# Performance work log

Hardware: AMD Instinct MI355X
Metric: run time of the kernel (lower is better)

## Reference

```python
import jax, jax.numpy as jnp
import numpy as np
import math

N, T, D = 4096, 32, 158
NEWS, DGRU = 1024, 128
G, E, H, K = 8, 8, 4, 2          # groups, experts/group, heads, top_k
HID = G * E                       # 64
DH = E // H                       # head_dim = 2
NEG = -1e30


def setup_inputs() -> dict:
    key = jax.random.key(0)
    ks = jax.random.split(key, 16)
    s = 0.05
    price_feature = jax.random.normal(ks[0], (N, T, D), jnp.float32)
    news_feature = jax.random.normal(ks[1], (N, T, NEWS), jnp.float32)
    news_mask = jax.random.uniform(ks[2], (N, T), dtype=jnp.float32)
    # simple deterministic router params (stand-in for injected router module)
    router_W = jax.random.normal(ks[3], (D + NEWS, DGRU), jnp.float32) * s
    router_b = jnp.zeros((DGRU,), jnp.float32)
    # hidden_to_gate: Linear(d_gru -> hidden_dim)
    gate_W = jax.random.normal(ks[4], (DGRU, HID), jnp.float32) * s
    gate_b = jnp.zeros((HID,), jnp.float32)
    # 64 tiny experts: Linear(hidden_dim -> 1), stacked [G,E,HID]
    expert_W = jax.random.normal(ks[5], (G, E, HID), jnp.float32) * s
    expert_b = jnp.zeros((G, E), jnp.float32)
    # per-group attention weights, torch Linear layout [out,in] -> [G,E,E]
    wq = jax.random.normal(ks[6], (G, E, E), jnp.float32) * s
    wk = jax.random.normal(ks[7], (G, E, E), jnp.float32) * s
    wv = jax.random.normal(ks[8], (G, E, E), jnp.float32) * s
    wo = jax.random.normal(ks[9], (G, E, E), jnp.float32) * s
    wq_b = jnp.zeros((G, E), jnp.float32)
    wk_b = jnp.zeros((G, E), jnp.float32)
    wv_b = jnp.zeros((G, E), jnp.float32)
    wo_b = jnp.zeros((G, E), jnp.float32)
    return dict(price_feature=price_feature, news_feature=news_feature, news_mask=news_mask,
                router_W=router_W, router_b=router_b, gate_W=gate_W, gate_b=gate_b,
                expert_W=expert_W, expert_b=expert_b,
                wq=wq, wq_b=wq_b, wk=wk, wk_b=wk_b, wv=wv, wv_b=wv_b, wo=wo, wo_b=wo_b)


def _forward(price_feature, news_feature, news_mask, router_W, router_b,
             gate_W, gate_b, expert_W, expert_b,
             wq, wq_b, wk, wk_b, wv, wv_b, wo, wo_b):
    n = price_feature.shape[0]
    # ---- router: masked temporal pooling + linear + tanh -> [N, d_gru]
    m = news_mask[:, :, None]
    news_agg = (news_feature * m).sum(1) / jnp.clip(m.sum(1), 1e-6)
    price_agg = price_feature.mean(1)
    h = jnp.tanh(jnp.concatenate([price_agg, news_agg], axis=-1) @ router_W + router_b)
    # ---- gate: [N, HID]
    hidden = h @ gate_W + gate_b
    # ---- top-k routing with scatter mask + masked softmax
    top_k_values, top_k_indices = jax.lax.top_k(hidden, K)
    mask = jnp.zeros_like(hidden).at[jnp.arange(n)[:, None], top_k_indices].set(1.0)
    masked_hidden = jnp.where(mask == 0, NEG, hidden)
    routing_weights = jax.nn.softmax(masked_hidden, axis=1)  # [N, HID]
    # ---- all 64 experts at once: [N, G, E]
    expert_out = jnp.einsum('nh,geh->nge', hidden, expert_W) + expert_b
    # ---- inner-group attention (faithful to torch view/transpose layout)
    q = jnp.einsum('nge,gfe->ngf', expert_out, wq) + wq_b
    k = jnp.einsum('nge,gfe->ngf', expert_out, wk) + wk_b
    v = jnp.einsum('nge,gfe->ngf', expert_out, wv) + wv_b
    # view [N,G,H,DH] then transpose(1,2) -> attend over DH positions, H as features
    qt = q.reshape(n, G, H, DH).transpose(0, 1, 3, 2)  # [N,G,DH,H]
    kt = k.reshape(n, G, H, DH).transpose(0, 1, 3, 2)
    vt = v.reshape(n, G, H, DH).transpose(0, 1, 3, 2)
    scores = jnp.einsum('ngdh,ngeh->ngde', qt, kt) / math.sqrt(DH)  # [N,G,DH,DH]
    attn = jax.nn.softmax(scores, axis=-1)
    attended = jnp.einsum('ngde,ngeh->ngdh', attn, vt)  # [N,G,DH,H]
    attended = attended.transpose(0, 1, 3, 2).reshape(n, G, E)
    agg = jnp.einsum('nge,gfe->ngf', attended, wo) + wo_b  # [N,G,E]
    all_outputs = agg.reshape(n, HID)
    weighted = all_outputs * routing_weights
    predictions = weighted.sum(axis=1)  # [N]
    return predictions, routing_weights, hidden, top_k_indices, routing_weights


def reference(price_feature, news_feature, news_mask, router_W, router_b,
              gate_W, gate_b, expert_W, expert_b,
              wq, wq_b, wk, wk_b, wv, wv_b, wo, wo_b):
    return _forward(price_feature, news_feature, news_mask, router_W, router_b,
                    gate_W, gate_b, expert_W, expert_b,
                    wq, wq_b, wk, wk_b, wv, wv_b, wo, wo_b)
```

## Files before the change

### kernel.cpp

```cpp
#include <hip/hip_runtime.h>
#include <math.h>

namespace {

constexpr int TT    = 32;
constexpr int DD    = 158;
constexpr int NEWSC = 1024;
constexpr int XDIM  = 1182;
constexpr int XPAD  = 1184;
constexpr int DGRU  = 128;
constexpr int HIDN  = 64;
constexpr int RPB   = 8;
constexpr int SPLIT = 592;

__global__ __launch_bounds__(256, 2)
void miga_fused(const float* __restrict__ price,
                const float* __restrict__ news,
                const float* __restrict__ mask,
                const float* __restrict__ rW,
                const float* __restrict__ rb,
                const float* __restrict__ gW,
                const float* __restrict__ gb,
                const float* __restrict__ eW,
                const float* __restrict__ eb,
                const float* __restrict__ wq,
                const float* __restrict__ wqb,
                const float* __restrict__ wk,
                const float* __restrict__ wkb,
                const float* __restrict__ wv,
                const float* __restrict__ wvb,
                const float* __restrict__ wo,
                const float* __restrict__ wob,
                float* __restrict__ out, int nrows)
{
  __shared__ __align__(16) float xs[RPB][XPAD];
  __shared__ float hs[RPB][DGRU];
  __shared__ float part[RPB][DGRU];
  __shared__ float hid_s[RPB][HIDN];
  __shared__ float eo_s[RPB][HIDN];
  __shared__ float q_s[RPB][HIDN];
  __shared__ float k_s[RPB][HIDN];
  __shared__ float v_s[RPB][HIDN];
  __shared__ float att_s[RPB][HIDN];
  __shared__ float den_m[RPB];

  float* eWt = &xs[0][0];

  const int tid  = threadIdx.x;
  const int row0 = blockIdx.x * RPB;

  if (tid < RPB) {
    float s = 0.f;
    #pragma unroll
    for (int t = 0; t < TT; ++t) s += mask[(size_t)(row0 + tid) * TT + t];
    den_m[tid] = fmaxf(s, 1e-6f);
  }

  if (tid < DD) {
    for (int r = 0; r < RPB; ++r) {
      const float* pr = price + ((size_t)(row0 + r) * TT) * DD + tid;
      float acc = 0.f;
      #pragma unroll
      for (int t = 0; t < TT; ++t) acc += pr[(size_t)t * DD];
      xs[r][tid] = acc * (1.0f / (float)TT);
    }
  }
  __syncthreads();

  {
    const int j0 = tid * 4;
    for (int r = 0; r < RPB; ++r) {
      const float* nb = news + ((size_t)(row0 + r) * TT) * NEWSC + j0;
      const float* mb = mask + (size_t)(row0 + r) * TT;
      float ax = 0.f, ay = 0.f, az = 0.f, aw = 0.f;
      #pragma unroll 4
      for (int t = 0; t < TT; ++t) {
        const float  mv = mb[t];
        const float4 nv = *(const float4*)(nb + (size_t)t * NEWSC);
        ax += mv * nv.x; ay += mv * nv.y; az += mv * nv.z; aw += mv * nv.w;
      }
      const float dn = den_m[r];
      xs[r][DD + j0 + 0] = ax / dn;
      xs[r][DD + j0 + 1] = ay / dn;
      xs[r][DD + j0 + 2] = az / dn;
      xs[r][DD + j0 + 3] = aw / dn;
    }
  }
  __syncthreads();

  {
    const int sh = tid >> 7;
    const int o  = tid & 127;
    const int ib = sh ? SPLIT : 0;
    const int ie = sh ? XDIM : SPLIT;
    float acc[RPB];
    #pragma unroll
    for (int r = 0; r < RPB; ++r) acc[r] = 0.f;
    int i0 = ib;
    for (; i0 + 8 <= ie; i0 += 8) {
      const float w0 = rW[(size_t)(i0 + 0) * DGRU + o];
      const float w1 = rW[(size_t)(i0 + 1) * DGRU + o];
      const float w2 = rW[(size_t)(i0 + 2) * DGRU + o];
      const float w3 = rW[(size_t)(i0 + 3) * DGRU + o];
      const float w4 = rW[(size_t)(i0 + 4) * DGRU + o];
      const float w5 = rW[(size_t)(i0 + 5) * DGRU + o];
      const float w6 = rW[(size_t)(i0 + 6) * DGRU + o];
      const float w7 = rW[(size_t)(i0 + 7) * DGRU + o];
      #pragma unroll
      for (int r = 0; r < RPB; ++r) {
        const float4 xa = *(const float4*)&xs[r][i0];
        const float4 xb = *(const float4*)&xs[r][i0 + 4];
        acc[r] += xa.x * w0 + xa.y * w1 + xa.z * w2 + xa.w * w3
                + xb.x * w4 + xb.y * w5 + xb.z * w6 + xb.w * w7;
      }
    }
    for (; i0 < ie; ++i0) {
      const float w = rW[(size_t)i0 * DGRU + o];
      #pragma unroll
      for (int r = 0; r < RPB; ++r) acc[r] += xs[r][i0] * w;
    }
    if (sh) {
      #pragma unroll
      for (int r = 0; r < RPB; ++r) part[r][o] = acc[r];
    }
    __syncthreads();
    if (!sh) {
      const float b = rb[o];
      #pragma unroll
      for (int r = 0; r < RPB; ++r) hs[r][o] = tanhf(acc[r] + part[r][o] + b);
    }
    #pragma unroll
    for (int kk = 0; kk < 16; ++kk) {
      const int f  = tid + 256 * kk;
      const int ge = f >> 6;
      const int j  = f & 63;
      eWt[j * 65 + ge] = eW[f];
    }
  }
  __syncthreads();

  const int wgi = tid >> 6;
  const int ln  = tid & 63;
  const int ra  = wgi;
  const int rb2 = wgi + 4;

  float h0 = gb[ln], h1 = gb[ln];
  #pragma unroll 4
  for (int i = 0; i < DGRU; ++i) {
    const float w = gW[(size_t)i * HIDN + ln];
    h0 += hs[ra][i]  * w;
    h1 += hs[rb2][i] * w;
  }
  hid_s[ra][ln]  = h0;
  hid_s[rb2][ln] = h1;
  __syncthreads();

  float* out_pred = out;
  float* out_rw1  = out + (size_t)nrows;
  float* out_hid  = out + (size_t)nrows * 65;
  float* out_idx  = out + (size_t)nrows * 129;
  float* out_rw2  = out + (size_t)nrows * 131;

  const float hvv[2] = {h0, h1};
  int   i1v[2], i2v[2];
  float w1v[2], w2v[2];
  #pragma unroll
  for (int rr = 0; rr < 2; ++rr) {
    const int r   = wgi + rr * 4;
    const int row = row0 + r;
    const float hv = hvv[rr];
    float bv = hv; int bi = ln;
    #pragma unroll
    for (int off = 32; off >= 1; off >>= 1) {
      const float ov = __shfl_xor(bv, off);
      const int   oi = __shfl_xor(bi, off);
      if (ov > bv || (ov == bv && oi < bi)) { bv = ov; bi = oi; }
    }
    float cv = (ln == bi) ? -1e30f : hv; int ci = ln;
    #pragma unroll
    for (int off = 32; off >= 1; off >>= 1) {
      const float ov = __shfl_xor(cv, off);
      const int   oi = __shfl_xor(ci, off);
      if (ov > cv || (ov == cv && oi < ci)) { cv = ov; ci = oi; }
    }
    const float e2 = expf(cv - bv);
    const float zi = 1.0f / (1.0f + e2);
    const float rwl = (ln == bi) ? zi : (ln == ci) ? e2 * zi : 0.0f;
    out_hid[(size_t)row * 64 + ln] = hv;
    out_rw1[(size_t)row * 64 + ln] = rwl;
    out_rw2[(size_t)row * 64 + ln] = rwl;
    if (ln < 2) out_idx[(size_t)row * 2 + ln] = (float)(ln == 0 ? bi : ci);
    i1v[rr] = bi; i2v[rr] = ci; w1v[rr] = zi; w2v[rr] = e2 * zi;
  }

  {
    float a0 = eb[ln], a1 = eb[ln];
    #pragma unroll 4
    for (int j = 0; j < HIDN; ++j) {
      const float w = eWt[j * 65 + ln];
      a0 += hid_s[ra][j]  * w;
      a1 += hid_s[rb2][j] * w;
    }
    eo_s[ra][ln]  = a0;
    eo_s[rb2][ln] = a1;
  }
  __syncthreads();

  const int gg = ln >> 3;
  #pragma unroll
  for (int rr = 0; rr < 2; ++rr) {
    const int r = wgi + rr * 4;
    float aq = wqb[ln], ak = wkb[ln], av = wvb[ln];
    #pragma unroll
    for (int ee = 0; ee < 8; ++ee) {
      const float xv = eo_s[r][gg * 8 + ee];
      aq += xv * wq[ln * 8 + ee];
      ak += xv * wk[ln * 8 + ee];
      av += xv * wv[ln * 8 + ee];
    }
    q_s[r][ln] = aq; k_s[r][ln] = ak; v_s[r][ln] = av;
  }
  __syncthreads();

  {
    const int e8  = ln & 7;
    const int dd2 = e8 & 1;
    const int hh  = e8 >> 1;
    const float rs2 = 0.7071067811865476f;
    #pragma unroll
    for (int rr = 0; rr < 2; ++rr) {
      const int r = wgi + rr * 4;
      float s0 = 0.f, s1 = 0.f;
      #pragma unroll
      for (int h2 = 0; h2 < 4; ++h2) {
        const float qv = q_s[r][gg * 8 + h2 * 2 + dd2];
        s0 += qv * k_s[r][gg * 8 + h2 * 2 + 0];
        s1 += qv * k_s[r][gg * 8 + h2 * 2 + 1];
      }
      s0 *= rs2; s1 *= rs2;
      const float mx = fmaxf(s0, s1);
      const float a0 = expf(s0 - mx);
      const float a1 = expf(s1 - mx);
      const float zi = 1.0f / (a0 + a1);
      att_s[r][ln] = (a0 * v_s[r][gg * 8 + hh * 2 + 0]
                    + a1 * v_s[r][gg * 8 + hh * 2 + 1]) * zi;
    }
  }
  __syncthreads();

  #pragma unroll
  for (int rr = 0; rr < 2; ++rr) {
    const int r   = wgi + rr * 4;
    const int row = row0 + r;
    float acc = wob[ln];
    #pragma unroll
    for (int ee = 0; ee < 8; ++ee)
      acc += att_s[r][gg * 8 + ee] * wo[ln * 8 + ee];
    const float rwl = (ln == i1v[rr]) ? w1v[rr] : (ln == i2v[rr]) ? w2v[rr] : 0.0f;
    float ps = acc * rwl;
    #pragma unroll
    for (int off = 32; off >= 1; off >>= 1) ps += __shfl_xor(ps, off);
    if (ln == 0) out_pred[row] = ps;
  }
}

}

extern "C" void kernel_launch(void* const* d_in, const int* in_sizes, int n_in,
                              void* d_out, int out_size, void* d_ws, size_t ws_size,
                              hipStream_t stream) {
  const float* price = (const float*)d_in[0];
  const float* news  = (const float*)d_in[1];
  const float* mask  = (const float*)d_in[2];
  const float* rW    = (const float*)d_in[3];
  const float* rb    = (const float*)d_in[4];
  const float* gW    = (const float*)d_in[5];
  const float* gb    = (const float*)d_in[6];
  const float* eW    = (const float*)d_in[7];
  const float* eb    = (const float*)d_in[8];
  const float* wq    = (const float*)d_in[9];
  const float* wqb   = (const float*)d_in[10];
  const float* wk    = (const float*)d_in[11];
  const float* wkb   = (const float*)d_in[12];
  const float* wv    = (const float*)d_in[13];
  const float* wvb   = (const float*)d_in[14];
  const float* wo    = (const float*)d_in[15];
  const float* wob   = (const float*)d_in[16];
  float* out = (float*)d_out;
  const int nrows = in_sizes[2] / TT;
  (void)d_ws; (void)ws_size; (void)out_size; (void)n_in;
  miga_fused<<<dim3(nrows / RPB), dim3(256), 0, stream>>>(
      price, news, mask, rW, rb, gW, gb, eW, eb,
      wq, wqb, wk, wkb, wv, wvb, wo, wob, out, nrows);
}
```

Measured before the change: 800.2 us.

## Split pooling into separate bandwidth-bound kernel and read pooled features from workspace

Moves masked temporal pooling of news and price features into a separate kernel with one block per row, writing pooled features to a workspace buffer. The MoE/router kernel then reads pooled rows from global memory instead of a large shared-memory tile. The expert weight transpose into shared memory is replaced by direct float4 global reads. This raises parallelism and occupancy for the memory-heavy stage, at the cost of an extra global write and read of the pooled features and a second launch.

```diff
diff --git a/kernel.cpp b/kernel.cpp
--- a/kernel.cpp
+++ b/kernel.cpp
@@ -6,17 +6,56 @@
 constexpr int TT    = 32;
 constexpr int DD    = 158;
 constexpr int NEWSC = 1024;
-constexpr int XDIM  = 1182;
 constexpr int XPAD  = 1184;
+constexpr int NOFF  = 160;
 constexpr int DGRU  = 128;
 constexpr int HIDN  = 64;
 constexpr int RPB   = 8;
-constexpr int SPLIT = 592;
-
-__global__ __launch_bounds__(256, 2)
-void miga_fused(const float* __restrict__ price,
+
+__global__ __launch_bounds__(256)
+void agg_kernel(const float* __restrict__ price,
                 const float* __restrict__ news,
                 const float* __restrict__ mask,
+                float* __restrict__ x)
+{
+  const int r   = blockIdx.x;
+  const int tid = threadIdx.x;
+  __shared__ float m_s[TT];
+
+  if (tid < TT) m_s[tid] = mask[(size_t)r * TT + tid];
+  __syncthreads();
+
+  float den = 0.f;
+  #pragma unroll
+  for (int t = 0; t < TT; ++t) den += m_s[t];
+  den = fmaxf(den, 1e-6f);
+  const float rden = 1.0f / den;
+
+  {
+    const int j0 = tid * 4;
+    const float* nb = news + (size_t)r * TT * NEWSC + j0;
+    float ax = 0.f, ay = 0.f, az = 0.f, aw = 0.f;
+    #pragma unroll
+    for (int t = 0; t < TT; ++t) {
+      const float  mv = m_s[t];
+      const float4 nv = *(const float4*)(nb + (size_t)t * NEWSC);
+      ax += mv * nv.x; ay += mv * nv.y; az += mv * nv.z; aw += mv * nv.w;
+    }
+    float4 o4 = make_float4(ax * rden, ay * rden, az * rden, aw * rden);
+    *(float4*)(x + (size_t)r * XPAD + NOFF + j0) = o4;
+  }
+
+  if (tid < DD) {
+    const float* pr = price + (size_t)r * TT * DD + tid;
+    float acc = 0.f;
+    #pragma unroll
+    for (int t = 0; t < TT; ++t) acc += pr[(size_t)t * DD];
+    x[(size_t)r * XPAD + tid] = acc * (1.0f / (float)TT);
+  }
+}
+
+__global__ __launch_bounds__(256)
+void moe_kernel(const float* __restrict__ x,
                 const float* __restrict__ rW,
                 const float* __restrict__ rb,
                 const float* __restrict__ gW,
@@ -33,7 +72,6 @@
                 const float* __restrict__ wob,
                 float* __restrict__ out, int nrows)
 {
-  __shared__ __align__(16) float xs[RPB][XPAD];
   __shared__ float hs[RPB][DGRU];
   __shared__ float part[RPB][DGRU];
   __shared__ float hid_s[RPB][HIDN];
@@ -42,83 +80,49 @@
   __shared__ float k_s[RPB][HIDN];
   __shared__ float v_s[RPB][HIDN];
   __shared__ float att_s[RPB][HIDN];
-  __shared__ float den_m[RPB];
-
-  float* eWt = &xs[0][0];
 
   const int tid  = threadIdx.x;
   const int row0 = blockIdx.x * RPB;
 
-  if (tid < RPB) {
-    float s = 0.f;
-    #pragma unroll
-    for (int t = 0; t < TT; ++t) s += mask[(size_t)(row0 + tid) * TT + t];
-    den_m[tid] = fmaxf(s, 1e-6f);
-  }
-
-  if (tid < DD) {
-    for (int r = 0; r < RPB; ++r) {
-      const float* pr = price + ((size_t)(row0 + r) * TT) * DD + tid;
-      float acc = 0.f;
-      #pragma unroll
-      for (int t = 0; t < TT; ++t) acc += pr[(size_t)t * DD];
-      xs[r][tid] = acc * (1.0f / (float)TT);
-    }
-  }
-  __syncthreads();
-
-  {
-    const int j0 = tid * 4;
-    for (int r = 0; r < RPB; ++r) {
-      const float* nb = news + ((size_t)(row0 + r) * TT) * NEWSC + j0;
-      const float* mb = mask + (size_t)(row0 + r) * TT;
-      float ax = 0.f, ay = 0.f, az = 0.f, aw = 0.f;
-      #pragma unroll 4
-      for (int t = 0; t < TT; ++t) {
-        const float  mv = mb[t];
-        const float4 nv = *(const float4*)(nb + (size_t)t * NEWSC);
-        ax += mv * nv.x; ay += mv * nv.y; az += mv * nv.z; aw += mv * nv.w;
-      }
-      const float dn = den_m[r];
-      xs[r][DD + j0 + 0] = ax / dn;
-      xs[r][DD + j0 + 1] = ay / dn;
-      xs[r][DD + j0 + 2] = az / dn;
-      xs[r][DD + j0 + 3] = aw / dn;
-    }
-  }
-  __syncthreads();
-
   {
     const int sh = tid >> 7;
     const int o  = tid & 127;
-    const int ib = sh ? SPLIT : 0;
-    const int ie = sh ? XDIM : SPLIT;
     float acc[RPB];
     #pragma unroll
     for (int r = 0; r < RPB; ++r) acc[r] = 0.f;
-    int i0 = ib;
-    for (; i0 + 8 <= ie; i0 += 8) {
-      const float w0 = rW[(size_t)(i0 + 0) * DGRU + o];
-      const float w1 = rW[(size_t)(i0 + 1) * DGRU + o];
-      const float w2 = rW[(size_t)(i0 + 2) * DGRU + o];
-      const float w3 = rW[(size_t)(i0 + 3) * DGRU + o];
-      const float w4 = rW[(size_t)(i0 + 4) * DGRU + o];
-      const float w5 = rW[(size_t)(i0 + 5) * DGRU + o];
-      const float w6 = rW[(size_t)(i0 + 6) * DGRU + o];
-      const float w7 = rW[(size_t)(i0 + 7) * DGRU + o];
-      #pragma unroll
-      for (int r = 0; r < RPB; ++r) {
-        const float4 xa = *(const float4*)&xs[r][i0];
-        const float4 xb = *(const float4*)&xs[r][i0 + 4];
-        acc[r] += xa.x * w0 + xa.y * w1 + xa.z * w2 + xa.w * w3
-                + xb.x * w4 + xb.y * w5 + xb.z * w6 + xb.w * w7;
+
+    const float* xb = x + (size_t)row0 * XPAD;
+
+    auto seg = [&](int b, int e, int xbase, int wbase) {
+      int i = b;
+      for (; i + 8 <= e; i += 8) {
+        float w[8];
+        #pragma unroll
+        for (int kk = 0; kk < 8; ++kk)
+          w[kk] = rW[(size_t)(wbase + i + kk) * DGRU + o];
+        #pragma unroll
+        for (int r = 0; r < RPB; ++r) {
+          const float* xr = xb + (size_t)r * XPAD + xbase + i;
+          acc[r] += xr[0] * w[0] + xr[1] * w[1] + xr[2] * w[2] + xr[3] * w[3]
+                  + xr[4] * w[4] + xr[5] * w[5] + xr[6] * w[6] + xr[7] * w[7];
+        }
       }
-    }
-    for (; i0 < ie; ++i0) {
-      const float w = rW[(size_t)i0 * DGRU + o];
-      #pragma unroll
-      for (int r = 0; r < RPB; ++r) acc[r] += xs[r][i0] * w;
-    }
+      for (; i < e; ++i) {
+        const float w = rW[(size_t)(wbase + i) * DGRU + o];
+        #pragma unroll
+        for (int r = 0; r < RPB; ++r)
+          acc[r] += xb[(size_t)r * XPAD + xbase + i] * w;
+      }
+    };
+
+    if (!sh) {
+      seg(0, 80, 0, 0);
+      seg(0, 512, NOFF, DD);
+    } else {
+      seg(80, DD, 0, 0);
+      seg(512, NEWSC, NOFF, DD);
+    }
+
     if (sh) {
       #pragma unroll
       for (int r = 0; r < RPB; ++r) part[r][o] = acc[r];
@@ -128,13 +132,6 @@
       const float b = rb[o];
       #pragma unroll
       for (int r = 0; r < RPB; ++r) hs[r][o] = tanhf(acc[r] + part[r][o] + b);
-    }
-    #pragma unroll
-    for (int kk = 0; kk < 16; ++kk) {
-      const int f  = tid + 256 * kk;
-      const int ge = f >> 6;
-      const int j  = f & 63;
-      eWt[j * 65 + ge] = eW[f];
     }
   }
   __syncthreads();
@@ -195,11 +192,15 @@
 
   {
     float a0 = eb[ln], a1 = eb[ln];
-    #pragma unroll 4
-    for (int j = 0; j < HIDN; ++j) {
-      const float w = eWt[j * 65 + ln];
-      a0 += hid_s[ra][j]  * w;
-      a1 += hid_s[rb2][j] * w;
+    const float4* ew4 = (const float4*)(eW + (size_t)ln * HIDN);
+    #pragma unroll
+    for (int c = 0; c < 16; ++c) {
+      const float4 w4 = ew4[c];
+      const int j = c * 4;
+      a0 += hid_s[ra][j]  * w4.x + hid_s[ra][j+1]  * w4.y
+          + hid_s[ra][j+2]  * w4.z + hid_s[ra][j+3]  * w4.w;
+      a1 += hid_s[rb2][j] * w4.x + hid_s[rb2][j+1] * w4.y
+          + hid_s[rb2][j+2] * w4.z + hid_s[rb2][j+3] * w4.w;
     }
     eo_s[ra][ln]  = a0;
     eo_s[rb2][ln] = a1;
@@ -287,9 +288,12 @@
   const float* wo    = (const float*)d_in[15];
   const float* wob   = (const float*)d_in[16];
   float* out = (float*)d_out;
+  float* xws = (float*)d_ws;
   const int nrows = in_sizes[2] / TT;
-  (void)d_ws; (void)ws_size; (void)out_size; (void)n_in;
-  miga_fused<<<dim3(nrows / RPB), dim3(256), 0, stream>>>(
-      price, news, mask, rW, rb, gW, gb, eW, eb,
+  (void)out_size; (void)n_in; (void)ws_size;
+
+  agg_kernel<<<dim3(nrows), dim3(256), 0, stream>>>(price, news, mask, xws);
+  moe_kernel<<<dim3(nrows / RPB), dim3(256), 0, stream>>>(
+      xws, rW, rb, gW, gb, eW, eb,
       wq, wqb, wk, wkb, wv, wvb, wo, wob, out, nrows);
 }
```

New measurement: 835.2 us. 4.4% more time.
